# Performance work log

Hardware: AMD Instinct MI355X
Metric: run time of the kernel (lower is better)

## Reference

```python
import jax, jax.numpy as jnp
from jax import lax
import numpy as np

H, W, C_IN, C_OUT, K, GROUPS, EPS = 1024, 1024, 64, 128, 3, 32, 1e-5


def setup_inputs() -> dict:
    key = jax.random.key(0)
    k = jax.random.split(key, 7)
    # flax Conv default kernel init (lecun_normal) scale approximated; exact init values
    # don't matter for a correctness baseline, only shapes/math.
    x = jax.random.normal(k[0], (H, W, C_IN), dtype=jnp.float32)
    W1 = jax.random.normal(k[1], (K, K, C_IN, C_OUT), dtype=jnp.float32) * (1.0 / np.sqrt(K * K * C_IN))
    b1 = jnp.zeros((C_OUT,), dtype=jnp.float32)
    W2 = jax.random.normal(k[2], (1, 1, C_IN, C_OUT), dtype=jnp.float32) * (1.0 / np.sqrt(C_IN))
    b2 = jnp.zeros((C_OUT,), dtype=jnp.float32)
    gn_scale = jnp.ones((C_OUT,), dtype=jnp.float32)
    gn_bias = jnp.zeros((C_OUT,), dtype=jnp.float32)
    return {"x": x, "W1": W1, "b1": b1, "W2": W2, "b2": b2,
            "gn_scale": gn_scale, "gn_bias": gn_bias}


def _forward(x, W1, b1, W2, b2, gn_scale, gn_bias):
    nx, ny = x.shape[0], x.shape[1]
    # NOTE: linspace spans [0, nx] inclusive (one past last valid index nx-1),
    # matching the original; map_coordinates order=1 zero-fills out of range.
    coords = jnp.meshgrid(jnp.linspace(0, nx, nx // 2), jnp.linspace(0, ny, ny // 2))
    x = jax.vmap(jax.scipy.ndimage.map_coordinates, in_axes=(-1, None, None), out_axes=-1)(x, coords, 1)
    # dual conv (SAME padding, stride 1), unbatched -> add/remove batch dim
    xb = x[None]  # [1, h, w, C_IN]
    dn = ('NHWC', 'HWIO', 'NHWC')
    y1 = lax.conv_general_dilated(xb, W1, (1, 1), 'SAME', dimension_numbers=dn) + b1
    y2 = lax.conv_general_dilated(xb, W2, (1, 1), 'SAME', dimension_numbers=dn) + b2
    y = (y1 + y2)[0]  # [h, w, C_OUT]
    # GroupNorm (flax default: 32 groups, eps=1e-5, scale+bias)
    h, w, c = y.shape
    yg = y.reshape(h, w, GROUPS, c // GROUPS)
    mu = yg.mean(axis=(0, 1, 3), keepdims=True)
    var = yg.var(axis=(0, 1, 3), keepdims=True)
    yn = ((yg - mu) * lax.rsqrt(var + EPS)).reshape(h, w, c)
    return jax.nn.gelu(yn * gn_scale + gn_bias)  # flax gelu: approximate=True


def reference(x, W1, b1, W2, b2, gn_scale, gn_bias):
    return _forward(x, W1, b1, W2, b2, gn_scale, gn_bias)
```

## Files before the change

### kernel.cpp

```cpp
#include <hip/hip_runtime.h>
#include <math.h>

#define HI 1024
#define WI 1024
#define HO 512
#define WO 512
#define CIN 64
#define COUT 128
#define NW (9*CIN*COUT)

typedef __attribute__((ext_vector_type(8))) short bf16x8;
typedef __attribute__((ext_vector_type(4))) float f32x4;


__device__ __forceinline__ unsigned short f2bf(float f) {
    unsigned u = __float_as_uint(f);
    u += 0x7fffu + ((u >> 16) & 1u);
    return (unsigned short)(u >> 16);
}

__global__ void k_pack(const float* __restrict__ W1, const float* __restrict__ b1,
                       const float* __restrict__ W2, const float* __restrict__ b2,
                       unsigned short* __restrict__ Bpk, float* __restrict__ bf) {
    int idx = blockIdx.x * 256 + threadIdx.x;
    if (idx < NW) {
        int j  = idx & 7;
        int l  = (idx >> 3) & 63;
        int nf = (idx >> 9) & 7;
        int h  = (idx >> 12) & 1;
        int t  = idx >> 13;
        int cin  = (h << 5) + ((l >> 4) << 3) + j;
        int cout = (nf << 4) + (l & 15);
        float v = W1[(t * 64 + cin) * 128 + cout];
        if (t == 4) v += W2[cin * 128 + cout];
        Bpk[idx] = f2bf(v);
    } else if (idx < NW + COUT) {
        int c = idx - NW;
        bf[c] = b1[c] + b2[c];
    }
}

__global__ __launch_bounds__(512, 4) void k_conv(
        const float* __restrict__ x,
        const unsigned short* __restrict__ Bpk,
        const float* __restrict__ bf,
        unsigned short* __restrict__ yb, float* __restrict__ part) {
    __shared__ short lxs[324 * 64];
    __shared__ float sred[8][32];

    const int tid = threadIdx.x;
    const int l   = tid & 63;
    const int w   = tid >> 6;
    const int gr0 = (blockIdx.x >> 5) << 4;
    const int gc0 = (blockIdx.x & 31) << 4;

    const float step = 1024.0f / 511.0f;
    #pragma unroll
    for (int k = 0; k < 6; ++k) {
        int idx = tid + (k << 9);
        if (idx < 324 * 8) {
            int pos = idx >> 3, c = idx & 7;
            int row = pos / 18;
            int col = pos - row * 18;
            int gr = gr0 + row - 1, gc = gc0 + col - 1;
            float a0 = 0.f, a1 = 0.f, a2 = 0.f, a3 = 0.f;
            float a4 = 0.f, a5 = 0.f, a6 = 0.f, a7 = 0.f;
            if (gr >= 0 && gr < HO && gc >= 0 && gc < WO) {
                float tr = (float)gc * step;
                float tc = (float)gr * step;
                int r0 = (int)tr; float fr = tr - (float)r0;
                int c0 = (int)tc; float fc = tc - (float)c0;
                float w00 = (1.f - fr) * (1.f - fc);
                float w01 = (1.f - fr) * fc;
                float w10 = fr * (1.f - fc);
                float w11 = fr * fc;
                const float* xb = x + (c << 3);
                #define TAP(R, C, W) \
                    if ((R) < HI && (C) < WI) { \
                        const float* p = xb + ((((R) << 10) + (C)) << 6); \
                        float4 v0 = *(const float4*)p; \
                        float4 v1 = *(const float4*)(p + 4); \
                        a0 += (W) * v0.x; a1 += (W) * v0.y; a2 += (W) * v0.z; a3 += (W) * v0.w; \
                        a4 += (W) * v1.x; a5 += (W) * v1.y; a6 += (W) * v1.z; a7 += (W) * v1.w; \
                    }
                TAP(r0,     c0,     w00)
                TAP(r0,     c0 + 1, w01)
                TAP(r0 + 1, c0,     w10)
                TAP(r0 + 1, c0 + 1, w11)
                #undef TAP
            }
            uint4 pk;
            pk.x = (unsigned)f2bf(a0) | ((unsigned)f2bf(a1) << 16);
            pk.y = (unsigned)f2bf(a2) | ((unsigned)f2bf(a3) << 16);
            pk.z = (unsigned)f2bf(a4) | ((unsigned)f2bf(a5) << 16);
            pk.w = (unsigned)f2bf(a6) | ((unsigned)f2bf(a7) << 16);
            *(uint4*)((char*)lxs + pos * 128 + ((c ^ (col & 7)) << 4)) = pk;
        }
    }

    const int wq  = w & 3;
    const int wh  = w >> 2;
    const int wr0 = (wq >> 1) << 3;
    const int wc0 = (wq & 1) << 3;
    const int qg  = l >> 4;
    const int p15 = l & 15;
    const int colbase = wc0 + (l & 7);
    int rowbase[4];
    #pragma unroll
    for (int mf = 0; mf < 4; ++mf)
        rowbase[mf] = (wr0 + 2 * mf + (p15 >> 3)) * 18 + colbase;

    f32x4 acc[4][4];
    #pragma unroll
    for (int nf = 0; nf < 4; ++nf) {
        f32x4 b4 = *(const f32x4*)&bf[(wh << 6) + (nf << 4) + (qg << 2)];
        #pragma unroll
        for (int mf = 0; mf < 4; ++mf)
            acc[mf][nf] = b4;
    }

    const bf16x8* Bbase = (const bf16x8*)Bpk;
    bf16x8 bcur[4];
    #pragma unroll
    for (int nf = 0; nf < 4; ++nf)
        bcur[nf] = Bbase[(((wh << 2) + nf) << 6) + l];

    __syncthreads();

    #pragma unroll 1
    for (int th = 0; th < 18; ++th) {
        const int thn = (th < 17) ? th + 1 : 0;
        bf16x8 bnxt[4];
        {
            const bf16x8* Bth = Bbase + (thn << 9);
            #pragma unroll
            for (int nf = 0; nf < 4; ++nf)
                bnxt[nf] = Bth[(((wh << 2) + nf) << 6) + l];
        }
        const int t  = th >> 1;
        const int h  = th & 1;
        const int dy = (t * 11) >> 5;
        const int dx = t - dy * 3;
        const int chunkx = ((h << 2) + qg) ^ ((colbase + dx) & 7);
        bf16x8 a[4];
        #pragma unroll
        for (int mf = 0; mf < 4; ++mf)
            a[mf] = *(const bf16x8*)((const char*)lxs +
                     (rowbase[mf] + dy * 18 + dx) * 128 + (chunkx << 4));
        #pragma unroll
        for (int mf = 0; mf < 4; ++mf) {
            #pragma unroll
            for (int nf = 0; nf < 4; ++nf)
                acc[mf][nf] = __builtin_amdgcn_mfma_f32_16x16x32_bf16(
                    bcur[nf], a[mf], acc[mf][nf], 0, 0, 0);
        }
        #pragma unroll
        for (int nf = 0; nf < 4; ++nf)
            bcur[nf] = bnxt[nf];
    }

    float s[4], s2[4];
    #pragma unroll
    for (int nf = 0; nf < 4; ++nf) { s[nf] = 0.f; s2[nf] = 0.f; }
    #pragma unroll
    for (int mf = 0; mf < 4; ++mf) {
        int gr = gr0 + wr0 + (mf << 1) + (p15 >> 3);
        int gc = gc0 + wc0 + (p15 & 7);
        unsigned short* op = yb + (((gr << 9) + gc) << 7) + (wh << 6) + (qg << 2);
        #pragma unroll
        for (int nf = 0; nf < 4; ++nf) {
            f32x4 v = acc[mf][nf];
            ushort4 o;
            o.x = f2bf(v[0]); o.y = f2bf(v[1]); o.z = f2bf(v[2]); o.w = f2bf(v[3]);
            *(ushort4*)(op + (nf << 4)) = o;
            s[nf]  += v[0] + v[1] + v[2] + v[3];
            s2[nf] += v[0] * v[0] + v[1] * v[1] + v[2] * v[2] + v[3] * v[3];
        }
    }
    #pragma unroll
    for (int nf = 0; nf < 4; ++nf) {
        s[nf]  += __shfl_xor(s[nf], 1);  s[nf]  += __shfl_xor(s[nf], 2);
        s[nf]  += __shfl_xor(s[nf], 4);  s[nf]  += __shfl_xor(s[nf], 8);
        s2[nf] += __shfl_xor(s2[nf], 1); s2[nf] += __shfl_xor(s2[nf], 2);
        s2[nf] += __shfl_xor(s2[nf], 4); s2[nf] += __shfl_xor(s2[nf], 8);
    }
    if (p15 == 0) {
        #pragma unroll
        for (int nf = 0; nf < 4; ++nf) {
            sred[w][(nf << 2) + qg]      = s[nf];
            sred[w][16 + (nf << 2) + qg] = s2[nf];
        }
    }
    __syncthreads();
    if (tid < 64) {
        int isS2 = tid >> 5;
        int g    = tid & 31;
        int gh   = g >> 4;
        int g16  = (g & 15) + (isS2 << 4);
        float v = sred[(gh << 2) + 0][g16] + sred[(gh << 2) + 1][g16]
                + sred[(gh << 2) + 2][g16] + sred[(gh << 2) + 3][g16];
        part[(blockIdx.x << 6) + (isS2 << 5) + g] = v;
    }
}

__global__ void k_final(const float* __restrict__ part, float* __restrict__ params) {
    __shared__ float sh[256];
    int t = threadIdx.x;
    int col = t & 63, q = t >> 6;
    float s = 0.f;
    for (int r = q; r < 1024; r += 4) s += part[r * 64 + col];
    sh[t] = s;
    __syncthreads();
    if (t < 64) sh[t] = sh[t] + sh[64 + t] + sh[128 + t] + sh[192 + t];
    __syncthreads();
    if (t < 32) {
        const float invN = 1.0f / (512.0f * 512.0f * 4.0f);
        float mu  = sh[t] * invN;
        float var = sh[32 + t] * invN - mu * mu;
        params[t]      = mu;
        params[32 + t] = rsqrtf(var + 1e-5f);
    }
}

__global__ void k_gelu(const unsigned short* __restrict__ yb, float* __restrict__ out,
                       const float* __restrict__ params, const float* __restrict__ scale,
                       const float* __restrict__ bias) {
    int t = blockIdx.x * 256 + threadIdx.x;
    int c0 = (t & 15) << 3;
    uint4 raw = ((const uint4*)yb)[t];
    unsigned us[8];
    us[0] = raw.x & 0xffffu; us[1] = raw.x >> 16;
    us[2] = raw.y & 0xffffu; us[3] = raw.y >> 16;
    us[4] = raw.z & 0xffffu; us[5] = raw.z >> 16;
    us[6] = raw.w & 0xffffu; us[7] = raw.w >> 16;
    int g0 = c0 >> 2;
    float mu0 = params[g0],     iv0 = params[32 + g0];
    float mu1 = params[g0 + 1], iv1 = params[33 + g0];
    float scb[8], bib[8];
    *(float4*)&scb[0] = *(const float4*)&scale[c0];
    *(float4*)&scb[4] = *(const float4*)&scale[c0 + 4];
    *(float4*)&bib[0] = *(const float4*)&bias[c0];
    *(float4*)&bib[4] = *(const float4*)&bias[c0 + 4];
    float o[8];
    #pragma unroll
    for (int k = 0; k < 8; ++k) {
        float xf = __uint_as_float(us[k] << 16);
        float mu = (k < 4) ? mu0 : mu1;
        float iv = (k < 4) ? iv0 : iv1;
        float z  = (xf - mu) * iv * scb[k] + bib[k];
        float a  = 0.7978845608028654f * (z + 0.044715f * z * z * z);
        o[k] = z / (1.0f + __expf(-2.0f * a));
    }
    float4* op = (float4*)(out + ((size_t)t << 3));
    op[0] = make_float4(o[0], o[1], o[2], o[3]);
    op[1] = make_float4(o[4], o[5], o[6], o[7]);
}

extern "C" void kernel_launch(void* const* d_in, const int* in_sizes, int n_in,
                              void* d_out, int out_size, void* d_ws, size_t ws_size,
                              hipStream_t stream) {
    const float* x  = (const float*)d_in[0];
    const float* W1 = (const float*)d_in[1];
    const float* b1 = (const float*)d_in[2];
    const float* W2 = (const float*)d_in[3];
    const float* b2 = (const float*)d_in[4];
    const float* gs = (const float*)d_in[5];
    const float* gb = (const float*)d_in[6];
    float* out = (float*)d_out;

    char* ws = (char*)d_ws;
    unsigned short* yb  = (unsigned short*)(ws);
    unsigned short* Bpk = (unsigned short*)(ws + 67108864);
    float* bf           = (float*)(ws + 67256320);
    float* part         = (float*)(ws + 67256832);
    float* params       = (float*)(ws + 67518976);

    k_pack<<<(NW + COUT + 255) / 256, 256, 0, stream>>>(W1, b1, W2, b2, Bpk, bf);
    k_conv<<<1024, 512, 0, stream>>>(x, Bpk, bf, yb, part);
    k_final<<<1, 256, 0, stream>>>(part, params);
    k_gelu<<<(HO * WO * COUT / 8) / 256, 256, 0, stream>>>(yb, out, params, gs, gb);
}
```

Measured before the change: 212.4 us.

## Precompute bf16 downsampled input and stage conv halo via global_load_lds

Moves the bilinear resampling out of the conv kernel into a separate k_down pass that writes a bf16 512x512x64 image into the output buffer as scratch. The conv kernel then fills its 18x18 halo tile with direct global-to-LDS loads, pointing out-of-range pixels at a small zero buffer, so each block no longer recomputes interpolation for its halo. This trades an extra kernel launch and an extra write and read of the intermediate image for removing redundant interpolation work and register staging in the conv prologue.

After: 218.7 us. 1.03x slower.

```diff
diff --git a/kernel.cpp b/kernel.cpp
--- a/kernel.cpp
+++ b/kernel.cpp
@@ -13,6 +13,10 @@
 typedef __attribute__((ext_vector_type(4))) float f32x4;
 
 
+#define GLDS(g, l) __builtin_amdgcn_global_load_lds( \
+    (const __attribute__((address_space(1))) void*)(g), \
+    (__attribute__((address_space(3))) void*)(l), 16, 0, 0)
+
 __device__ __forceinline__ unsigned short f2bf(float f) {
     unsigned u = __float_as_uint(f);
     u += 0x7fffu + ((u >> 16) & 1u);
@@ -21,7 +25,8 @@
 
 __global__ void k_pack(const float* __restrict__ W1, const float* __restrict__ b1,
                        const float* __restrict__ W2, const float* __restrict__ b2,
-                       unsigned short* __restrict__ Bpk, float* __restrict__ bf) {
+                       unsigned short* __restrict__ Bpk, float* __restrict__ bf,
+                       unsigned short* __restrict__ zeroz) {
     int idx = blockIdx.x * 256 + threadIdx.x;
     if (idx < NW) {
         int j  = idx & 7;
@@ -37,13 +42,48 @@
     } else if (idx < NW + COUT) {
         int c = idx - NW;
         bf[c] = b1[c] + b2[c];
-    }
+    } else if (idx < NW + COUT + 64) {
+        zeroz[idx - NW - COUT] = 0;
+    }
+}
+
+__global__ void k_down(const float* __restrict__ x, unsigned short* __restrict__ xd) {
+    int t = blockIdx.x * 256 + threadIdx.x;
+    if (t >= HO * WO * (CIN / 4)) return;
+    int c4 = t & 15;
+    int j  = (t >> 4) & (WO - 1);
+    int i  = t >> 13;
+    const float step = 1024.0f / 511.0f;
+    float tr = (float)j * step;
+    float tc = (float)i * step;
+    int r0 = (int)tr; float fr = tr - (float)r0;
+    int c0 = (int)tc; float fc = tc - (float)c0;
+    float w00 = (1.f - fr) * (1.f - fc);
+    float w01 = (1.f - fr) * fc;
+    float w10 = fr * (1.f - fc);
+    float w11 = fr * fc;
+    float4 acc = make_float4(0.f, 0.f, 0.f, 0.f);
+    int cc = c4 << 2;
+    #define TAP(R, C, W) \
+        if ((R) < HI && (C) < WI) { \
+            const float4 v = *(const float4*)&x[(((R) << 10) + (C)) * CIN + cc]; \
+            acc.x += (W) * v.x; acc.y += (W) * v.y; acc.z += (W) * v.z; acc.w += (W) * v.w; \
+        }
+    TAP(r0,     c0,     w00)
+    TAP(r0,     c0 + 1, w01)
+    TAP(r0 + 1, c0,     w10)
+    TAP(r0 + 1, c0 + 1, w11)
+    #undef TAP
+    ushort4 o;
+    o.x = f2bf(acc.x); o.y = f2bf(acc.y); o.z = f2bf(acc.z); o.w = f2bf(acc.w);
+    *(ushort4*)&xd[(((i << 9) + j) * CIN) + cc] = o;
 }
 
 __global__ __launch_bounds__(512, 4) void k_conv(
-        const float* __restrict__ x,
+        const unsigned short* __restrict__ xd,
         const unsigned short* __restrict__ Bpk,
         const float* __restrict__ bf,
+        const unsigned short* __restrict__ zeroz,
         unsigned short* __restrict__ yb, float* __restrict__ part) {
     __shared__ short lxs[324 * 64];
     __shared__ float sred[8][32];
@@ -54,55 +94,33 @@
     const int gr0 = (blockIdx.x >> 5) << 4;
     const int gc0 = (blockIdx.x & 31) << 4;
 
-    const float step = 1024.0f / 511.0f;
+    const int wq  = w & 3;
+    const int wh  = w >> 2;
+    const int qg  = l >> 4;
+    const bf16x8* Bbase = (const bf16x8*)Bpk;
+    bf16x8 bcur[4];
+    #pragma unroll
+    for (int nf = 0; nf < 4; ++nf)
+        bcur[nf] = Bbase[(((wh << 2) + nf) << 6) + l];
+    f32x4 bias4 = *(const f32x4*)&bf[(wh << 6) + (qg << 2)];
+
     #pragma unroll
     for (int k = 0; k < 6; ++k) {
         int idx = tid + (k << 9);
-        if (idx < 324 * 8) {
-            int pos = idx >> 3, c = idx & 7;
-            int row = pos / 18;
-            int col = pos - row * 18;
-            int gr = gr0 + row - 1, gc = gc0 + col - 1;
-            float a0 = 0.f, a1 = 0.f, a2 = 0.f, a3 = 0.f;
-            float a4 = 0.f, a5 = 0.f, a6 = 0.f, a7 = 0.f;
-            if (gr >= 0 && gr < HO && gc >= 0 && gc < WO) {
-                float tr = (float)gc * step;
-                float tc = (float)gr * step;
-                int r0 = (int)tr; float fr = tr - (float)r0;
-                int c0 = (int)tc; float fc = tc - (float)c0;
-                float w00 = (1.f - fr) * (1.f - fc);
-                float w01 = (1.f - fr) * fc;
-                float w10 = fr * (1.f - fc);
-                float w11 = fr * fc;
-                const float* xb = x + (c << 3);
-                #define TAP(R, C, W) \
-                    if ((R) < HI && (C) < WI) { \
-                        const float* p = xb + ((((R) << 10) + (C)) << 6); \
-                        float4 v0 = *(const float4*)p; \
-                        float4 v1 = *(const float4*)(p + 4); \
-                        a0 += (W) * v0.x; a1 += (W) * v0.y; a2 += (W) * v0.z; a3 += (W) * v0.w; \
-                        a4 += (W) * v1.x; a5 += (W) * v1.y; a6 += (W) * v1.z; a7 += (W) * v1.w; \
-                    }
-                TAP(r0,     c0,     w00)
-                TAP(r0,     c0 + 1, w01)
-                TAP(r0 + 1, c0,     w10)
-                TAP(r0 + 1, c0 + 1, w11)
-                #undef TAP
-            }
-            uint4 pk;
-            pk.x = (unsigned)f2bf(a0) | ((unsigned)f2bf(a1) << 16);
-            pk.y = (unsigned)f2bf(a2) | ((unsigned)f2bf(a3) << 16);
-            pk.z = (unsigned)f2bf(a4) | ((unsigned)f2bf(a5) << 16);
-            pk.w = (unsigned)f2bf(a6) | ((unsigned)f2bf(a7) << 16);
-            *(uint4*)((char*)lxs + pos * 128 + ((c ^ (col & 7)) << 4)) = pk;
-        }
-    }
-
-    const int wq  = w & 3;
-    const int wh  = w >> 2;
+        int pos = idx >> 3, c = idx & 7;
+        int row = (pos * 57) >> 10;
+        int col = pos - row * 18;
+        int gr = gr0 + row - 1, gc = gc0 + col - 1;
+        bool inpx = (gr >= 0) && (gr < HO) && (gc >= 0) && (gc < WO);
+        const unsigned short* src = inpx
+            ? xd + (((gr << 9) + gc) << 6) + ((c ^ (col & 7)) << 3)
+            : zeroz;
+        if (idx < 324 * 8)
+            GLDS(src, (char*)lxs + (((w << 6) + (k << 9)) << 4));
+    }
+
     const int wr0 = (wq >> 1) << 3;
     const int wc0 = (wq & 1) << 3;
-    const int qg  = l >> 4;
     const int p15 = l & 15;
     const int colbase = wc0 + (l & 7);
     int rowbase[4];
@@ -113,17 +131,10 @@
     f32x4 acc[4][4];
     #pragma unroll
     for (int nf = 0; nf < 4; ++nf) {
-        f32x4 b4 = *(const f32x4*)&bf[(wh << 6) + (nf << 4) + (qg << 2)];
         #pragma unroll
         for (int mf = 0; mf < 4; ++mf)
-            acc[mf][nf] = b4;
-    }
-
-    const bf16x8* Bbase = (const bf16x8*)Bpk;
-    bf16x8 bcur[4];
-    #pragma unroll
-    for (int nf = 0; nf < 4; ++nf)
-        bcur[nf] = Bbase[(((wh << 2) + nf) << 6) + l];
+            acc[mf][nf] = bias4;
+    }
 
     __syncthreads();
 
@@ -269,14 +280,17 @@
     float* out = (float*)d_out;
 
     char* ws = (char*)d_ws;
-    unsigned short* yb  = (unsigned short*)(ws);
-    unsigned short* Bpk = (unsigned short*)(ws + 67108864);
-    float* bf           = (float*)(ws + 67256320);
-    float* part         = (float*)(ws + 67256832);
-    float* params       = (float*)(ws + 67518976);
-
-    k_pack<<<(NW + COUT + 255) / 256, 256, 0, stream>>>(W1, b1, W2, b2, Bpk, bf);
-    k_conv<<<1024, 512, 0, stream>>>(x, Bpk, bf, yb, part);
+    unsigned short* xd    = (unsigned short*)d_out;
+    unsigned short* yb    = (unsigned short*)(ws);
+    unsigned short* Bpk   = (unsigned short*)(ws + 67108864);
+    float* bf             = (float*)(ws + 67256320);
+    float* part           = (float*)(ws + 67256832);
+    float* params         = (float*)(ws + 67518976);
+    unsigned short* zeroz = (unsigned short*)(ws + 67519232);
+
+    k_pack<<<(NW + COUT + 64 + 255) / 256, 256, 0, stream>>>(W1, b1, W2, b2, Bpk, bf, zeroz);
+    k_down<<<(HO * WO * (CIN / 4)) / 256, 256, 0, stream>>>(x, xd);
+    k_conv<<<1024, 512, 0, stream>>>(xd, Bpk, bf, zeroz, yb, part);
     k_final<<<1, 256, 0, stream>>>(part, params);
     k_gelu<<<(HO * WO * COUT / 8) / 256, 256, 0, stream>>>(yb, out, params, gs, gb);
 }
```

## Precompute downsampled bf16 input in prep kernel and read conv operands from global

Applied to the files above, without the earlier changes.

Moves the bilinear resampling of the input out of the conv kernel into a separate prep pass that writes a bf16 downsampled image, stored temporarily in the output buffer, plus a zeroed guard region. The conv kernel drops its shared-memory halo tile and loads A fragments straight from global/L2, using a fast interior path and a guarded edge path that redirects out-of-range taps to the zero guard. Blocks are remapped so each XCD handles contiguous rows for L2 locality. This removes the halo recomputation and LDS footprint but adds a full extra pass over the intermediate and relies on cache hits for repeated tap loads.

New measurement: 262.4 us. 23.5% more time.

```diff
diff --git a/kernel.cpp b/kernel.cpp
--- a/kernel.cpp
+++ b/kernel.cpp
@@ -8,6 +8,7 @@
 #define CIN 64
 #define COUT 128
 #define NW (9*CIN*COUT)
+#define GUARD_OFF 33554432
 
 typedef __attribute__((ext_vector_type(8))) short bf16x8;
 typedef __attribute__((ext_vector_type(4))) float f32x4;
@@ -19,145 +20,150 @@
     return (unsigned short)(u >> 16);
 }
 
-__global__ void k_pack(const float* __restrict__ W1, const float* __restrict__ b1,
+__global__ void k_prep(const float* __restrict__ x,
+                       const float* __restrict__ W1, const float* __restrict__ b1,
                        const float* __restrict__ W2, const float* __restrict__ b2,
+                       unsigned short* __restrict__ xd,
                        unsigned short* __restrict__ Bpk, float* __restrict__ bf) {
-    int idx = blockIdx.x * 256 + threadIdx.x;
-    if (idx < NW) {
-        int j  = idx & 7;
-        int l  = (idx >> 3) & 63;
-        int nf = (idx >> 9) & 7;
-        int h  = (idx >> 12) & 1;
-        int t  = idx >> 13;
-        int cin  = (h << 5) + ((l >> 4) << 3) + j;
-        int cout = (nf << 4) + (l & 15);
-        float v = W1[(t * 64 + cin) * 128 + cout];
-        if (t == 4) v += W2[cin * 128 + cout];
-        Bpk[idx] = f2bf(v);
-    } else if (idx < NW + COUT) {
-        int c = idx - NW;
-        bf[c] = b1[c] + b2[c];
+    int bid = blockIdx.x;
+    if (bid < 8192) {
+        int t = bid * 256 + threadIdx.x;
+        int c8 = t & 7;
+        int j  = (t >> 3) & (WO - 1);
+        int i  = t >> 12;
+        const float step = 1024.0f / 511.0f;
+        float tr = (float)j * step;
+        float tc = (float)i * step;
+        int r0 = (int)tr; float fr = tr - (float)r0;
+        int c0 = (int)tc; float fc = tc - (float)c0;
+        float w00 = (1.f - fr) * (1.f - fc);
+        float w01 = (1.f - fr) * fc;
+        float w10 = fr * (1.f - fc);
+        float w11 = fr * fc;
+        float a0 = 0.f, a1 = 0.f, a2 = 0.f, a3 = 0.f;
+        float a4 = 0.f, a5 = 0.f, a6 = 0.f, a7 = 0.f;
+        const float* xb = x + (c8 << 3);
+        #define TAP(R, C, W) \
+            if ((R) < HI && (C) < WI) { \
+                const float* p = xb + ((((R) << 10) + (C)) << 6); \
+                float4 v0 = *(const float4*)p; \
+                float4 v1 = *(const float4*)(p + 4); \
+                a0 += (W) * v0.x; a1 += (W) * v0.y; a2 += (W) * v0.z; a3 += (W) * v0.w; \
+                a4 += (W) * v1.x; a5 += (W) * v1.y; a6 += (W) * v1.z; a7 += (W) * v1.w; \
+            }
+        TAP(r0,     c0,     w00)
+        TAP(r0,     c0 + 1, w01)
+        TAP(r0 + 1, c0,     w10)
+        TAP(r0 + 1, c0 + 1, w11)
+        #undef TAP
+        uint4 pk;
+        pk.x = (unsigned)f2bf(a0) | ((unsigned)f2bf(a1) << 16);
+        pk.y = (unsigned)f2bf(a2) | ((unsigned)f2bf(a3) << 16);
+        pk.z = (unsigned)f2bf(a4) | ((unsigned)f2bf(a5) << 16);
+        pk.w = (unsigned)f2bf(a6) | ((unsigned)f2bf(a7) << 16);
+        *(uint4*)&xd[(((i << 9) + j) << 6) + (c8 << 3)] = pk;
+    } else {
+        int idx = (bid - 8192) * 256 + threadIdx.x;
+        if (idx < NW) {
+            int j  = idx & 7;
+            int l  = (idx >> 3) & 63;
+            int nf = (idx >> 9) & 7;
+            int h  = (idx >> 12) & 1;
+            int t  = idx >> 13;
+            int cin  = (h << 5) + ((l >> 4) << 3) + j;
+            int cout = (nf << 4) + (l & 15);
+            float v = W1[(t * 64 + cin) * 128 + cout];
+            if (t == 4) v += W2[cin * 128 + cout];
+            Bpk[idx] = f2bf(v);
+        } else if (idx < NW + COUT) {
+            int c = idx - NW;
+            bf[c] = b1[c] + b2[c];
+        } else if (idx < NW + COUT + 128) {
+            xd[(GUARD_OFF / 2) + (idx - NW - COUT)] = 0;
+        }
     }
 }
 
 __global__ __launch_bounds__(512, 4) void k_conv(
-        const float* __restrict__ x,
+        const unsigned short* __restrict__ xd,
         const unsigned short* __restrict__ Bpk,
         const float* __restrict__ bf,
         unsigned short* __restrict__ yb, float* __restrict__ part) {
-    __shared__ short lxs[324 * 64];
     __shared__ float sred[8][32];
 
     const int tid = threadIdx.x;
     const int l   = tid & 63;
     const int w   = tid >> 6;
-    const int gr0 = (blockIdx.x >> 5) << 4;
-    const int gc0 = (blockIdx.x & 31) << 4;
-
-    const float step = 1024.0f / 511.0f;
-    #pragma unroll
-    for (int k = 0; k < 6; ++k) {
-        int idx = tid + (k << 9);
-        if (idx < 324 * 8) {
-            int pos = idx >> 3, c = idx & 7;
-            int row = pos / 18;
-            int col = pos - row * 18;
-            int gr = gr0 + row - 1, gc = gc0 + col - 1;
-            float a0 = 0.f, a1 = 0.f, a2 = 0.f, a3 = 0.f;
-            float a4 = 0.f, a5 = 0.f, a6 = 0.f, a7 = 0.f;
-            if (gr >= 0 && gr < HO && gc >= 0 && gc < WO) {
-                float tr = (float)gc * step;
-                float tc = (float)gr * step;
-                int r0 = (int)tr; float fr = tr - (float)r0;
-                int c0 = (int)tc; float fc = tc - (float)c0;
-                float w00 = (1.f - fr) * (1.f - fc);
-                float w01 = (1.f - fr) * fc;
-                float w10 = fr * (1.f - fc);
-                float w11 = fr * fc;
-                const float* xb = x + (c << 3);
-                #define TAP(R, C, W) \
-                    if ((R) < HI && (C) < WI) { \
-                        const float* p = xb + ((((R) << 10) + (C)) << 6); \
-                        float4 v0 = *(const float4*)p; \
-                        float4 v1 = *(const float4*)(p + 4); \
-                        a0 += (W) * v0.x; a1 += (W) * v0.y; a2 += (W) * v0.z; a3 += (W) * v0.w; \
-                        a4 += (W) * v1.x; a5 += (W) * v1.y; a6 += (W) * v1.z; a7 += (W) * v1.w; \
-                    }
-                TAP(r0,     c0,     w00)
-                TAP(r0,     c0 + 1, w01)
-                TAP(r0 + 1, c0,     w10)
-                TAP(r0 + 1, c0 + 1, w11)
-                #undef TAP
-            }
-            uint4 pk;
-            pk.x = (unsigned)f2bf(a0) | ((unsigned)f2bf(a1) << 16);
-            pk.y = (unsigned)f2bf(a2) | ((unsigned)f2bf(a3) << 16);
-            pk.z = (unsigned)f2bf(a4) | ((unsigned)f2bf(a5) << 16);
-            pk.w = (unsigned)f2bf(a6) | ((unsigned)f2bf(a7) << 16);
-            *(uint4*)((char*)lxs + pos * 128 + ((c ^ (col & 7)) << 4)) = pk;
-        }
-    }
+    const int bid = blockIdx.x;
+    const int xcd  = bid & 7;
+    const int kk   = bid >> 3;
+    const int trow = (xcd << 2) + (kk >> 5);
+    const int tcol = kk & 31;
+    const int gr0 = trow << 4;
+    const int gc0 = tcol << 4;
 
     const int wq  = w & 3;
     const int wh  = w >> 2;
+    const int qg  = l >> 4;
+    const int p15 = l & 15;
     const int wr0 = (wq >> 1) << 3;
     const int wc0 = (wq & 1) << 3;
-    const int qg  = l >> 4;
-    const int p15 = l & 15;
-    const int colbase = wc0 + (l & 7);
-    int rowbase[4];
-    #pragma unroll
-    for (int mf = 0; mf < 4; ++mf)
-        rowbase[mf] = (wr0 + 2 * mf + (p15 >> 3)) * 18 + colbase;
+    const int pcol = gc0 + wc0 + (l & 7) - 1;
+    int prow[4], rowbyte[4];
+    #pragma unroll
+    for (int mf = 0; mf < 4; ++mf) {
+        prow[mf]    = gr0 + wr0 + 2 * mf + (p15 >> 3) - 1;
+        rowbyte[mf] = prow[mf] * 65536 + pcol * 128 + (qg << 4);
+    }
+    const char* xdc = (const char*)xd;
+    const bf16x8* Bbase = (const bf16x8*)Bpk;
 
     f32x4 acc[4][4];
-    #pragma unroll
-    for (int nf = 0; nf < 4; ++nf) {
-        f32x4 b4 = *(const f32x4*)&bf[(wh << 6) + (nf << 4) + (qg << 2)];
-        #pragma unroll
-        for (int mf = 0; mf < 4; ++mf)
-            acc[mf][nf] = b4;
-    }
-
-    const bf16x8* Bbase = (const bf16x8*)Bpk;
-    bf16x8 bcur[4];
-    #pragma unroll
-    for (int nf = 0; nf < 4; ++nf)
-        bcur[nf] = Bbase[(((wh << 2) + nf) << 6) + l];
-
-    __syncthreads();
-
-    #pragma unroll 1
-    for (int th = 0; th < 18; ++th) {
-        const int thn = (th < 17) ? th + 1 : 0;
-        bf16x8 bnxt[4];
-        {
-            const bf16x8* Bth = Bbase + (thn << 9);
-            #pragma unroll
-            for (int nf = 0; nf < 4; ++nf)
-                bnxt[nf] = Bth[(((wh << 2) + nf) << 6) + l];
-        }
-        const int t  = th >> 1;
-        const int h  = th & 1;
-        const int dy = (t * 11) >> 5;
-        const int dx = t - dy * 3;
-        const int chunkx = ((h << 2) + qg) ^ ((colbase + dx) & 7);
-        bf16x8 a[4];
-        #pragma unroll
-        for (int mf = 0; mf < 4; ++mf)
-            a[mf] = *(const bf16x8*)((const char*)lxs +
-                     (rowbase[mf] + dy * 18 + dx) * 128 + (chunkx << 4));
-        #pragma unroll
-        for (int mf = 0; mf < 4; ++mf) {
-            #pragma unroll
-            for (int nf = 0; nf < 4; ++nf)
-                acc[mf][nf] = __builtin_amdgcn_mfma_f32_16x16x32_bf16(
-                    bcur[nf], a[mf], acc[mf][nf], 0, 0, 0);
-        }
+    {
+        f32x4 bias4 = *(const f32x4*)&bf[(wh << 6) + (qg << 2)];
         #pragma unroll
         for (int nf = 0; nf < 4; ++nf)
-            bcur[nf] = bnxt[nf];
-    }
+            #pragma unroll
+            for (int mf = 0; mf < 4; ++mf)
+                acc[mf][nf] = bias4;
+    }
+
+    const bool edge = (trow == 0) | (trow == 31) | (tcol == 0) | (tcol == 31);
+
+#define TAPS(EDGE)                                                             \
+    _Pragma("unroll 1")                                                        \
+    for (int t = 0; t < 9; ++t) {                                              \
+        const int dy = (t * 11) >> 5;                                 \
+        const int dx = t - dy * 3;                                             \
+        const bf16x8* Bt = Bbase + (t << 10);                                  \
+        _Pragma("unroll")                                                      \
+        for (int h = 0; h < 2; ++h) {                                          \
+            bf16x8 b[4], a[4];                                                 \
+            _Pragma("unroll")                                                  \
+            for (int nf = 0; nf < 4; ++nf)                                     \
+                b[nf] = Bt[(h << 9) + (((wh << 2) + nf) << 6) + l];            \
+            _Pragma("unroll")                                                  \
+            for (int mf = 0; mf < 4; ++mf) {                                   \
+                int off = rowbyte[mf] + dy * 65536 + dx * 128 + (h << 6);      \
+                if (EDGE) {                                                    \
+                    bool vok = ((unsigned)(prow[mf] + dy) < 512u) &&           \
+                               ((unsigned)(pcol + dx) < 512u);                 \
+                    off = vok ? off : GUARD_OFF;                               \
+                }                                                              \
+                a[mf] = *(const bf16x8*)(xdc + off);                           \
+            }                                                                  \
+            _Pragma("unroll")                                                  \
+            for (int mf = 0; mf < 4; ++mf) {                                   \
+                _Pragma("unroll")                                              \
+                for (int nf = 0; nf < 4; ++nf)                                 \
+                    acc[mf][nf] = __builtin_amdgcn_mfma_f32_16x16x32_bf16(     \
+                        b[nf], a[mf], acc[mf][nf], 0, 0, 0);                   \
+            }                                                                  \
+        }                                                                      \
+    }
+
+    if (!edge) { TAPS(false) } else { TAPS(true) }
+#undef TAPS
 
     float s[4], s2[4];
     #pragma unroll
@@ -199,7 +205,7 @@
         int g16  = (g & 15) + (isS2 << 4);
         float v = sred[(gh << 2) + 0][g16] + sred[(gh << 2) + 1][g16]
                 + sred[(gh << 2) + 2][g16] + sred[(gh << 2) + 3][g16];
-        part[(blockIdx.x << 6) + (isS2 << 5) + g] = v;
+        part[(bid << 6) + (isS2 << 5) + g] = v;
     }
 }
 
@@ -269,14 +275,15 @@
     float* out = (float*)d_out;
 
     char* ws = (char*)d_ws;
+    unsigned short* xd  = (unsigned short*)d_out;
     unsigned short* yb  = (unsigned short*)(ws);
     unsigned short* Bpk = (unsigned short*)(ws + 67108864);
     float* bf           = (float*)(ws + 67256320);
     float* part         = (float*)(ws + 67256832);
     float* params       = (float*)(ws + 67518976);
 
-    k_pack<<<(NW + COUT + 255) / 256, 256, 0, stream>>>(W1, b1, W2, b2, Bpk, bf);
-    k_conv<<<1024, 512, 0, stream>>>(x, Bpk, bf, yb, part);
+    k_prep<<<8192 + 289, 256, 0, stream>>>(x, W1, b1, W2, b2, xd, Bpk, bf);
+    k_conv<<<1024, 512, 0, stream>>>(xd, Bpk, bf, yb, part);
     k_final<<<1, 256, 0, stream>>>(part, params);
     k_gelu<<<(HO * WO * COUT / 8) / 256, 256, 0, stream>>>(yb, out, params, gs, gb);
 }
```
